# Performance work log

Measured on AMD Instinct MI355X. Metric: run time of the kernel, lower is better.

The kernel has to match this reference:

```python
import jax, jax.numpy as jnp
import numpy as np
from jax import lax

B, C, H, W = 8, 512, 64, 64
K = 3            # dynamic depthwise kernel size
GROUPS = C       # n_groups defaults to in_channels (depthwise)
EPS = 1e-5


def setup_inputs() -> dict:
    key = jax.random.key(0)
    ks = jax.random.split(key, 6)
    x = jax.random.normal(ks[0], (B, C, H, W), dtype=jnp.float32)
    w_spatial = jax.random.normal(ks[1], (B, C, 1, K, K), dtype=jnp.float32) * 0.05
    w_pointwise = jax.random.normal(ks[2], (B, C, 1, 1, 1), dtype=jnp.float32) * 0.05
    bias = jax.random.normal(ks[3], (B, C), dtype=jnp.float32) * 0.05
    # shared final conv (nn.Conv2d(C, C, 3, reflect pad, bias=True))
    conv_w = jax.random.normal(ks[4], (C, C, 3, 3), dtype=jnp.float32) * 0.02
    conv_b = jax.random.normal(ks[5], (C,), dtype=jnp.float32) * 0.02
    return {"x": x, "w_spatial": w_spatial, "w_pointwise": w_pointwise,
            "bias": bias, "conv_w": conv_w, "conv_b": conv_b}


def _instance_norm(x):
    # F.instance_norm defaults: no affine, biased variance, eps=1e-5
    mu = jnp.mean(x, axis=(2, 3), keepdims=True)
    var = jnp.var(x, axis=(2, 3), keepdims=True)
    return (x - mu) * lax.rsqrt(var + EPS)


def _reflect_pad(x, p):
    return jnp.pad(x, ((0, 0), (0, 0), (p, p), (p, p)), mode="reflect")


def _conv(x, w, groups):
    return lax.conv_general_dilated(
        x, w, window_strides=(1, 1), padding="VALID",
        feature_group_count=groups,
        dimension_numbers=("NCHW", "OIHW", "NCHW"))


def _forward_single(xn, ws, wp, b):
    # xn: [C,H,W]; ws: [C,1,K,K]; wp: [C,1,1,1]; b: [C]
    p = (ws.shape[-1] - 1) // 2
    xp = _reflect_pad(xn[None], p)            # [1,C,H+2p,W+2p]
    y = _conv(xp, ws, GROUPS)                 # depthwise spatial conv
    y = _conv(y, wp, GROUPS)                  # grouped pointwise conv
    return (y + b[None, :, None, None])[0]    # [C,H,W]


def reference(x, w_spatial, w_pointwise, bias, conv_w, conv_b):
    xn = _instance_norm(x)
    mid = jax.vmap(_forward_single)(xn, w_spatial, w_pointwise, bias)  # [B,C,H,W]
    out = _conv(_reflect_pad(mid, 1), conv_w, 1) + conv_b[None, :, None, None]
    return out
```

## Files before the change

### kernel.cpp

```cpp
#include <hip/hip_runtime.h>
#include <hip/hip_bf16.h>


#define EPSV 1e-5f

typedef __attribute__((ext_vector_type(8))) short short8;
typedef __attribute__((ext_vector_type(4))) float f32x4;

__device__ __forceinline__ unsigned short f2bf(float f) {
  union { float f; unsigned int u; } v; v.f = f;
  unsigned int r = v.u + 0x7FFFu + ((v.u >> 16) & 1u);
  return (unsigned short)(r >> 16);
}

__device__ __forceinline__ int refl(int i, int n) {
  if (i < 0) i = -i;
  if (i >= n) i = 2 * n - 2 - i;
  return i;
}

__global__ __launch_bounds__(256) void k_stats(const float* __restrict__ x,
                                               float* __restrict__ mean,
                                               float* __restrict__ rstd) {
  int bc = blockIdx.x;
  const float4* xp = (const float4*)(x + (size_t)bc * 4096);
  int tid = threadIdx.x;
  float s = 0.f, q = 0.f;
#pragma unroll
  for (int k = 0; k < 4; ++k) {
    float4 v = xp[tid + k * 256];
    s += v.x + v.y + v.z + v.w;
    q += v.x * v.x + v.y * v.y + v.z * v.z + v.w * v.w;
  }
  __shared__ float s1[256], s2[256];
  s1[tid] = s; s2[tid] = q;
  __syncthreads();
  for (int st = 128; st > 0; st >>= 1) {
    if (tid < st) { s1[tid] += s1[tid + st]; s2[tid] += s2[tid + st]; }
    __syncthreads();
  }
  if (tid == 0) {
    float m = s1[0] * (1.f / 4096.f);
    float var = s2[0] * (1.f / 4096.f) - m * m;
    mean[bc] = m;
    rstd[bc] = rsqrtf(var + EPSV);
  }
}

__global__ __launch_bounds__(256) void k_wprep(const float* __restrict__ cw,
                                               unsigned short* __restrict__ wT2) {
  int idx = blockIdx.x * 256 + threadIdx.x;
  int e = idx & 7;
  int l15 = (idx >> 3) & 15;
  int g = (idx >> 7) & 3;
  int cq = (idx >> 9) & 15;
  int og = (idx >> 13) & 31;
  int t = idx >> 18;
  int o = og * 16 + l15;
  int c = cq * 32 + g * 8 + e;
  wT2[idx] = f2bf(cw[((size_t)(o * 512 + c)) * 9 + t]);
}

__global__ __launch_bounds__(256) void k_mid(const float* __restrict__ x,
                                             const float* __restrict__ wsp,
                                             const float* __restrict__ wpw,
                                             const float* __restrict__ bias,
                                             const float* __restrict__ mean,
                                             const float* __restrict__ rstd,
                                             unsigned short* __restrict__ mid) {
  int bid = blockIdx.x;
  int cg = bid & 3;
  int hq = (bid >> 2) & 15;
  int b = bid >> 6;
  int h0 = hq * 4;
  int tid = threadIdx.x;
  int cl = tid & 31, wq = tid >> 5;
  __shared__ float xs[32 * 391];

  int rowm[6];
#pragma unroll
  for (int r = 0; r < 6; ++r) rowm[r] = refl(h0 - 1 + r, 64);

  for (int cc = 0; cc < 4; ++cc) {
    int cbase = cg * 128 + cc * 32;
    __syncthreads();
#pragma unroll
    for (int k = 0; k < 12; ++k) {
      int idx = tid + k * 256;
      int c = idx / 96, rem = idx % 96;
      int r = rem >> 4, w4 = rem & 15;
      float4 v = *(const float4*)(x + ((size_t)(b * 512 + cbase + c)) * 4096 +
                                  rowm[r] * 64 + w4 * 4);
      float* dst = &xs[c * 391 + r * 65 + w4 * 4];
      dst[0] = v.x; dst[1] = v.y; dst[2] = v.z; dst[3] = v.w;
    }
    __syncthreads();

    int gc = b * 512 + cbase + cl;
    float m = mean[gc], rs = rstd[gc];
    float wp = wpw[gc], bv = bias[gc];
    float wk[9], wsum = 0.f;
#pragma unroll
    for (int t = 0; t < 9; ++t) { wk[t] = wsp[(size_t)gc * 9 + t]; wsum += wk[t]; }

    const float* xr = &xs[cl * 391];
#pragma unroll
    for (int r = 0; r < 4; ++r) {
#pragma unroll
      for (int wi = 0; wi < 8; ++wi) {
        int w = wq * 8 + wi;
        int wm = refl(w - 1, 64), wp1 = refl(w + 1, 64);
        float acc = 0.f;
#pragma unroll
        for (int dy = 0; dy < 3; ++dy) {
          const float* row = xr + (r + dy) * 65;
          acc += wk[dy * 3 + 0] * row[wm] + wk[dy * 3 + 1] * row[w] +
                 wk[dy * 3 + 2] * row[wp1];
        }
        float y = (acc - m * wsum) * rs;
        mid[(((size_t)(b * 64 + h0 + r)) * 64 + w) * 512 + cbase + cl] =
            f2bf(y * wp + bv);
      }
    }
  }
}

__global__ __launch_bounds__(512, 2) void k_conv(const unsigned short* __restrict__ wT2,
                                                 const unsigned short* __restrict__ mid,
                                                 const float* __restrict__ cb,
                                                 float* __restrict__ out) {
  int nbid = (blockIdx.x & 7) * 32 + (blockIdx.x >> 3);
  int mt = nbid >> 7;
  int b = (nbid >> 4) & 7;
  int h0 = (nbid & 15) * 4;
  int tid = threadIdx.x;
  int wid = tid >> 6, l = tid & 63;
  int wo = wid & 3, wn = wid >> 2;
  int l15 = l & 15, g = l >> 4;

  __shared__ union {
    unsigned short bbuf[2][6 * 64 * 32];
    float epi[64 * 132];
  } sm;

  int hrow_[6];
#pragma unroll
  for (int r = 0; r < 6; ++r) hrow_[r] = refl(h0 - 1 + r, 64);

  int boff[4][3];
#pragma unroll
  for (int ww = 0; ww < 4; ++ww)
#pragma unroll
    for (int dx = 0; dx < 3; ++dx) {
      int wr = refl(ww * 16 + l15 + dx - 1, 64);
      int s = g ^ ((wr >> 1) & 3);
      boff[ww][dx] = wr * 64 + s * 16;
    }

  f32x4 acc[4][8];
  f32x4 zero = {0.f, 0.f, 0.f, 0.f};
#pragma unroll
  for (int i = 0; i < 4; ++i)
#pragma unroll
    for (int j = 0; j < 8; ++j) acc[i][j] = zero;

  auto stageB = [&](int pi, int cc) {
    int cb32 = cc * 32;
    char* dstbase = (char*)&sm.bbuf[pi][0];
#pragma unroll
    for (int i = 0; i < 3; ++i) {
      int ld = tid + i * 512;
      int row = ld >> 8, rem = ld & 255, w = rem >> 2, s = rem & 3;
      int gcg = s ^ ((w >> 1) & 3);
      const unsigned short* src = mid +
          (((size_t)(b * 64 + hrow_[row])) * 64 + w) * 512 + cb32 + gcg * 8;
      __builtin_amdgcn_global_load_lds(
          (const __attribute__((address_space(1))) void*)src,
          (__attribute__((address_space(3))) void*)(dstbase + ld * 16),
          16, 0, 0);
    }
  };

  stageB(0, 0);

  const unsigned short* wa0 =
      wT2 + ((size_t)((mt * 16 + wo * 4) * 16)) * 512 + l * 8;

  for (int cc = 0; cc < 16; ++cc) {
    int pb = cc & 1;
    __syncthreads();
    if (cc < 15) stageB(pb ^ 1, cc + 1);
    const char* mb = (const char*)&sm.bbuf[pb][0];
    const unsigned short* wa = wa0 + (size_t)cc * 512;

#pragma unroll
    for (int t = 0; t < 9; ++t) {
      const int dy = t / 3, dx = t % 3;
      short8 a[4];
#pragma unroll
      for (int of = 0; of < 4; ++of)
        a[of] = *(const short8*)(wa + (size_t)t * 262144 + of * 8192);

      __builtin_amdgcn_s_setprio(1);
#pragma unroll
      for (int nf = 0; nf < 8; ++nf) {
        const int rowL = wn * 2 + (nf >> 2) + dy;
        short8 bf = *(const short8*)(mb + rowL * 4096 + boff[nf & 3][dx]);
#pragma unroll
        for (int of = 0; of < 4; ++of)
          acc[of][nf] = __builtin_amdgcn_mfma_f32_16x16x32_bf16(
              a[of], bf, acc[of][nf], 0, 0, 0);
      }
      __builtin_amdgcn_s_setprio(0);
    }
  }

#pragma unroll
  for (int p = 0; p < 4; ++p)
#pragma unroll
    for (int s = 0; s < 2; ++s) {
      __syncthreads();
      if (wo == p && wn == s) {
#pragma unroll
        for (int of = 0; of < 4; ++of)
#pragma unroll
          for (int nf = 0; nf < 8; ++nf) {
            int pix = (nf >> 2) * 64 + (nf & 3) * 16 + l15;
#pragma unroll
            for (int r = 0; r < 4; ++r) {
              int ol = of * 16 + g * 4 + r;
              sm.epi[ol * 132 + pix] = acc[of][nf][r];
            }
          }
      }
      __syncthreads();
#pragma unroll
      for (int it = 0; it < 4; ++it) {
        int idx = tid + it * 512;
        int ol = idx >> 5, rem = idx & 31;
        f32x4 v = *(const f32x4*)&sm.epi[ol * 132 + rem * 4];
        int o = mt * 256 + p * 64 + ol;
        float cbv = cb[o];
        v[0] += cbv; v[1] += cbv; v[2] += cbv; v[3] += cbv;
        int pix = rem * 4;
        int hh = h0 + s * 2 + (pix >> 6);
        int w4 = pix & 63;
        *(f32x4*)(out + (((size_t)(b * 512 + o)) * 64 + hh) * 64 + w4) = v;
      }
    }
}

extern "C" void kernel_launch(void* const* d_in, const int* in_sizes, int n_in,
                              void* d_out, int out_size, void* d_ws, size_t ws_size,
                              hipStream_t stream) {
  const float* x    = (const float*)d_in[0];
  const float* wsp  = (const float*)d_in[1];
  const float* wpw  = (const float*)d_in[2];
  const float* bias = (const float*)d_in[3];
  const float* cw   = (const float*)d_in[4];
  const float* cb   = (const float*)d_in[5];
  float* out = (float*)d_out;

  char* ws = (char*)d_ws;
  float* mean = (float*)ws;
  float* rstd = (float*)(ws + 16384);
  unsigned short* wT2 = (unsigned short*)(ws + 32768);
  unsigned short* mid = (unsigned short*)(ws + 32768 + 9 * 512 * 512 * 2);

  k_stats<<<4096, 256, 0, stream>>>(x, mean, rstd);
  k_wprep<<<9216, 256, 0, stream>>>(cw, wT2);
  k_mid<<<512, 256, 0, stream>>>(x, wsp, wpw, bias, mean, rstd, mid);
  k_conv<<<256, 512, 0, stream>>>(wT2, mid, cb, out);
}
```

Before: 176.0 us.

## Load conv B operands directly from global memory instead of LDS double-buffer

Removes the double-buffered LDS staging of the mid activation tile (global_load_lds plus per-chunk __syncthreads) in the main conv kernel. Each wave now reads its B fragments straight from global memory, relying on L1/L2 to absorb the 3x3 halo reuse. This drops the per-iteration barriers and the LDS traffic, but adds redundant global loads across waves, no explicit prefetch, and exposes more memory latency.

```diff
diff --git a/kernel.cpp b/kernel.cpp
--- a/kernel.cpp
+++ b/kernel.cpp
@@ -138,24 +138,19 @@
   int wo = wid & 3, wn = wid >> 2;
   int l15 = l & 15, g = l >> 4;
 
-  __shared__ union {
-    unsigned short bbuf[2][6 * 64 * 32];
-    float epi[64 * 132];
-  } sm;
-
-  int hrow_[6];
-#pragma unroll
-  for (int r = 0; r < 6; ++r) hrow_[r] = refl(h0 - 1 + r, 64);
-
-  int boff[4][3];
+  __shared__ float epi[64 * 132];
+
+  const unsigned short* rowb[4];
+#pragma unroll
+  for (int j = 0; j < 4; ++j)
+    rowb[j] = mid + ((size_t)(b * 64 + refl(h0 - 1 + wn * 2 + j, 64))) * 32768;
+
+  int goff[4][3];
 #pragma unroll
   for (int ww = 0; ww < 4; ++ww)
 #pragma unroll
-    for (int dx = 0; dx < 3; ++dx) {
-      int wr = refl(ww * 16 + l15 + dx - 1, 64);
-      int s = g ^ ((wr >> 1) & 3);
-      boff[ww][dx] = wr * 64 + s * 16;
-    }
+    for (int dx = 0; dx < 3; ++dx)
+      goff[ww][dx] = refl(ww * 16 + l15 + dx - 1, 64) * 512 + g * 8;
 
   f32x4 acc[4][8];
   f32x4 zero = {0.f, 0.f, 0.f, 0.f};
@@ -164,34 +159,12 @@
 #pragma unroll
     for (int j = 0; j < 8; ++j) acc[i][j] = zero;
 
-  auto stageB = [&](int pi, int cc) {
-    int cb32 = cc * 32;
-    char* dstbase = (char*)&sm.bbuf[pi][0];
-#pragma unroll
-    for (int i = 0; i < 3; ++i) {
-      int ld = tid + i * 512;
-      int row = ld >> 8, rem = ld & 255, w = rem >> 2, s = rem & 3;
-      int gcg = s ^ ((w >> 1) & 3);
-      const unsigned short* src = mid +
-          (((size_t)(b * 64 + hrow_[row])) * 64 + w) * 512 + cb32 + gcg * 8;
-      __builtin_amdgcn_global_load_lds(
-          (const __attribute__((address_space(1))) void*)src,
-          (__attribute__((address_space(3))) void*)(dstbase + ld * 16),
-          16, 0, 0);
-    }
-  };
-
-  stageB(0, 0);
-
   const unsigned short* wa0 =
       wT2 + ((size_t)((mt * 16 + wo * 4) * 16)) * 512 + l * 8;
 
   for (int cc = 0; cc < 16; ++cc) {
-    int pb = cc & 1;
-    __syncthreads();
-    if (cc < 15) stageB(pb ^ 1, cc + 1);
-    const char* mb = (const char*)&sm.bbuf[pb][0];
     const unsigned short* wa = wa0 + (size_t)cc * 512;
+    const int cb32 = cc * 32;
 
 #pragma unroll
     for (int t = 0; t < 9; ++t) {
@@ -200,17 +173,18 @@
 #pragma unroll
       for (int of = 0; of < 4; ++of)
         a[of] = *(const short8*)(wa + (size_t)t * 262144 + of * 8192);
+      short8 bf[8];
+#pragma unroll
+      for (int nf = 0; nf < 8; ++nf)
+        bf[nf] = *(const short8*)(rowb[(nf >> 2) + dy] + cb32 + goff[nf & 3][dx]);
 
       __builtin_amdgcn_s_setprio(1);
 #pragma unroll
-      for (int nf = 0; nf < 8; ++nf) {
-        const int rowL = wn * 2 + (nf >> 2) + dy;
-        short8 bf = *(const short8*)(mb + rowL * 4096 + boff[nf & 3][dx]);
+      for (int nf = 0; nf < 8; ++nf)
 #pragma unroll
         for (int of = 0; of < 4; ++of)
           acc[of][nf] = __builtin_amdgcn_mfma_f32_16x16x32_bf16(
-              a[of], bf, acc[of][nf], 0, 0, 0);
-      }
+              a[of], bf[nf], acc[of][nf], 0, 0, 0);
       __builtin_amdgcn_s_setprio(0);
     }
   }
@@ -229,7 +203,7 @@
 #pragma unroll
             for (int r = 0; r < 4; ++r) {
               int ol = of * 16 + g * 4 + r;
-              sm.epi[ol * 132 + pix] = acc[of][nf][r];
+              epi[ol * 132 + pix] = acc[of][nf][r];
             }
           }
       }
@@ -238,7 +212,7 @@
       for (int it = 0; it < 4; ++it) {
         int idx = tid + it * 512;
         int ol = idx >> 5, rem = idx & 31;
-        f32x4 v = *(const f32x4*)&sm.epi[ol * 132 + rem * 4];
+        f32x4 v = *(const f32x4*)&epi[ol * 132 + rem * 4];
         int o = mt * 256 + p * 64 + ol;
         float cbv = cb[o];
         v[0] += cbv; v[1] += cbv; v[2] += cbv; v[3] += cbv;
```

Result: slower. 393.6 us (+123.7%).
